# Optimization experiments

Hardware: AMD Instinct MI355X
Metric: run time of the kernel (lower is better)

## Reference

```python
import jax, jax.numpy as jnp
import numpy as np

B, S, D, H = 2, 2048, 2048, 16
HD = D // H


def setup_inputs() -> dict:
    key = jax.random.key(0)
    ks = jax.random.split(key, 9)
    scale = 0.02
    return {
        "x": jax.random.normal(ks[0], (B, S, D), dtype=jnp.float32),
        "wq_w": jax.random.normal(ks[1], (D, D), dtype=jnp.float32) * scale,
        "wq_b": jnp.zeros((D,), dtype=jnp.float32),
        "wk_w": jax.random.normal(ks[2], (D, D), dtype=jnp.float32) * scale,
        "wk_b": jnp.zeros((D,), dtype=jnp.float32),
        "wv_w": jax.random.normal(ks[3], (D, D), dtype=jnp.float32) * scale,
        "wv_b": jnp.zeros((D,), dtype=jnp.float32),
        "wo_w": jax.random.normal(ks[4], (D, D), dtype=jnp.float32) * scale,
        "wo_b": jnp.zeros((D,), dtype=jnp.float32),
    }


def reference(x, wq_w, wq_b, wk_w, wk_b, wv_w, wv_b, wo_w, wo_b):
    # torch Linear: y = x @ W.T + b
    q = x @ wq_w.T + wq_b  # [B,S,D]
    k = x @ wk_w.T + wk_b
    v = x @ wv_w.T + wv_b
    # [B,S,D] -> [B,H,S,HD]
    q = q.reshape(B, S, H, HD).transpose(0, 2, 1, 3)
    k = k.reshape(B, S, H, HD).transpose(0, 2, 1, 3)
    v = v.reshape(B, S, H, HD).transpose(0, 2, 1, 3)
    # scores [B,H,S,S], scaled by sqrt(d_dim) as in the original (not head_dim)
    scores = jnp.einsum("bhid,bhjd->bhij", q, k) / np.float32(np.sqrt(D))
    # faithful reproduction of the module's triu/transpose masking:
    m = jnp.swapaxes(jnp.triu(scores), -2, -1)  # lower-tri, zeros elsewhere
    p = jax.nn.softmax(m, axis=-2)              # softmax over dim=-2, zeros included
    a = jnp.swapaxes(jnp.triu(p), -2, -1)       # [B,H,S,S]
    attn = jnp.einsum("bhij,bhjd->bhid", a, v)  # [B,H,S,HD]
    concat = attn.transpose(0, 2, 1, 3).reshape(B, S, D)
    return concat @ wo_w.T + wo_b
```

## Files before the change

### kernel.cpp

```cpp
#include <hip/hip_runtime.h>

#define BB 2
#define SS 2048
#define DD 2048
#define HH 16
#define HDIM 128
#define MTOK (BB*SS)
#define BHH (BB*HH)
#define NCHUNK 16
#define QKN (2*DD)

typedef __attribute__((ext_vector_type(8))) __bf16 bf16x8;
typedef __attribute__((ext_vector_type(4))) float f32x4;
typedef __attribute__((ext_vector_type(8))) int i32x8;
typedef __attribute__((ext_vector_type(4))) int i32x4;

__device__ __forceinline__ unsigned short f2bf(float f) {
  unsigned u = __float_as_uint(f);
  u += 0x7FFFu + ((u >> 16) & 1u);
  return (unsigned short)(u >> 16);
}
__device__ __forceinline__ float bf2f(unsigned short s) {
  return __uint_as_float(((unsigned)s) << 16);
}
__device__ __forceinline__ unsigned char f2e4m3(float f) {
  int pk = __builtin_amdgcn_cvt_pk_fp8_f32(f, f, 0, false);
  return (unsigned char)(pk & 0xFF);
}

#define GLOAD_LDS16(src, dst)                                                   \
  __builtin_amdgcn_global_load_lds(                                             \
      (const void __attribute__((address_space(1)))*)(src),                     \
      (void __attribute__((address_space(3)))*)(dst), 16, 0, 0)

__global__ void cvt_x_dual(const float* __restrict__ in,
                           unsigned short* __restrict__ outb,
                           unsigned int* __restrict__ out8, int n4) {
  int i = blockIdx.x * blockDim.x + threadIdx.x;
  if (i < n4) {
    float4 v = ((const float4*)in)[i];
    ushort4 o;
    o.x = f2bf(v.x); o.y = f2bf(v.y); o.z = f2bf(v.z); o.w = f2bf(v.w);
    ((ushort4*)outb)[i] = o;
    int p0 = __builtin_amdgcn_cvt_pk_fp8_f32(v.x, v.y, 0, false);
    int p1 = __builtin_amdgcn_cvt_pk_fp8_f32(v.z, v.w, 0, false);
    out8[i] = (unsigned)(p0 & 0xFFFF) | ((unsigned)(p1 & 0xFFFF) << 16);
  }
}

__global__ void cvt_wqk8(const float* __restrict__ a, const float* __restrict__ b,
                         unsigned int* __restrict__ out) {
  int i = blockIdx.x * blockDim.x + threadIdx.x;
  int sel = i >> 20, r = i & 0xFFFFF;
  const float* src = sel == 0 ? a : b;
  float4 v = ((const float4*)src)[r];
  int p0 = __builtin_amdgcn_cvt_pk_fp8_f32(v.x, v.y, 0, false);
  int p1 = __builtin_amdgcn_cvt_pk_fp8_f32(v.z, v.w, 0, false);
  out[i] = (unsigned)(p0 & 0xFFFF) | ((unsigned)(p1 & 0xFFFF) << 16);
}

__global__ void cvt_w2bf(const float* __restrict__ a, const float* __restrict__ b,
                         unsigned short* __restrict__ out) {
  int i = blockIdx.x * blockDim.x + threadIdx.x;
  int sel = i >> 20, r = i & 0xFFFFF;
  const float* src = sel == 0 ? a : b;
  float4 v = ((const float4*)src)[r];
  ushort4 o;
  o.x = f2bf(v.x); o.y = f2bf(v.y); o.z = f2bf(v.z); o.w = f2bf(v.w);
  ((ushort4*)out)[i] = o;
}

__global__ void concat2(const float* __restrict__ a, const float* __restrict__ b,
                        float* __restrict__ out) {
  int i = blockIdx.x * blockDim.x + threadIdx.x;
  if (i < DD) { out[i] = a[i]; out[DD + i] = b[i]; }
}

template <bool OUT_BF16>
__global__ __launch_bounds__(256, 2) void gemm_bt(
    const __bf16* __restrict__ A, const __bf16* __restrict__ W,
    const float* __restrict__ bias, void* __restrict__ Cout,
    int M, int N, int K) {
  __shared__ __bf16 lA[128 * 32];
  __shared__ __bf16 lB[128 * 32];
  const int t = threadIdx.x;
  const int lane = t & 63, wave = t >> 6;
  const int quad = lane >> 4, l16 = lane & 15;
  const int m0 = blockIdx.y * 128, n0 = blockIdx.x * 128;
  const int wm = (wave & 1) * 64, wn = (wave >> 1) * 64;

  f32x4 acc[4][4] = {};

  for (int k0 = 0; k0 < K; k0 += 32) {
#pragma unroll
    for (int c = 0; c < 2; ++c) {
      int lin = c * 256 + t;
      int row = lin >> 2;
      int col = (lin & 3) * 8;
      const __bf16* srcA = A + (size_t)(m0 + row) * K + k0 + col;
      const __bf16* srcB = W + (size_t)(n0 + row) * K + k0 + col;
      GLOAD_LDS16(srcA, &lA[(c * 256 + wave * 64) * 8]);
      GLOAD_LDS16(srcB, &lB[(c * 256 + wave * 64) * 8]);
    }
    __syncthreads();
    bf16x8 af[4], bfr[4];
#pragma unroll
    for (int mt = 0; mt < 4; ++mt)
      af[mt] = *(const bf16x8*)&lA[(wm + mt * 16 + l16) * 32 + quad * 8];
#pragma unroll
    for (int nt = 0; nt < 4; ++nt)
      bfr[nt] = *(const bf16x8*)&lB[(wn + nt * 16 + l16) * 32 + quad * 8];
#pragma unroll
    for (int mt = 0; mt < 4; ++mt)
#pragma unroll
      for (int nt = 0; nt < 4; ++nt)
        acc[mt][nt] = __builtin_amdgcn_mfma_f32_16x16x32_bf16(af[mt], bfr[nt],
                                                              acc[mt][nt], 0, 0, 0);
    __syncthreads();
  }

#pragma unroll
  for (int mt = 0; mt < 4; ++mt) {
#pragma unroll
    for (int nt = 0; nt < 4; ++nt) {
      int col = n0 + wn + nt * 16 + l16;
      float bv = bias[col];
#pragma unroll
      for (int r = 0; r < 4; ++r) {
        int row = m0 + wm + mt * 16 + quad * 4 + r;
        float v = acc[mt][nt][r] + bv;
        if constexpr (OUT_BF16)
          ((unsigned short*)Cout)[(size_t)row * N + col] = f2bf(v);
        else
          ((float*)Cout)[(size_t)row * N + col] = v;
      }
    }
  }
}

__global__ __launch_bounds__(256, 2) void gemm_qk_fp8(
    const unsigned char* __restrict__ A8, const unsigned char* __restrict__ W8,
    const float* __restrict__ bias, unsigned char* __restrict__ Cout,
    int M, int N, int K) {
  __shared__ unsigned char lA[128 * 128];
  __shared__ unsigned char lB[128 * 128];
  const int t = threadIdx.x;
  const int lane = t & 63, wave = t >> 6;
  const int quad = lane >> 4, l16 = lane & 15;
  const int m0 = blockIdx.y * 128, n0 = blockIdx.x * 128;
  const int wm = (wave & 1) * 64, wn = (wave >> 1) * 64;
  const int p0 = (2 * quad) ^ (l16 & 7);

  f32x4 acc[4][4] = {};

  for (int k0 = 0; k0 < K; k0 += 128) {
#pragma unroll
    for (int c = 0; c < 4; ++c) {
      int lin = c * 256 + t;
      int row = lin >> 3;
      int ch = lin & 7;
      int sch = ch ^ (row & 7);
      const unsigned char* srcA = A8 + (size_t)(m0 + row) * K + k0 + sch * 16;
      const unsigned char* srcB = W8 + (size_t)(n0 + row) * K + k0 + sch * 16;
      GLOAD_LDS16(srcA, &lA[(c * 256 + wave * 64) * 16]);
      GLOAD_LDS16(srcB, &lB[(c * 256 + wave * 64) * 16]);
    }
    __syncthreads();
    i32x8 af[4];
#pragma unroll
    for (int mt = 0; mt < 4; ++mt) {
      int ra = (wm + mt * 16 + l16) * 128 + p0 * 16;
      ((i32x4*)&af[mt])[0] = *(const i32x4*)&lA[ra];
      ((i32x4*)&af[mt])[1] = *(const i32x4*)&lA[ra ^ 16];
    }
#pragma unroll
    for (int nt = 0; nt < 4; ++nt) {
      int rb = (wn + nt * 16 + l16) * 128 + p0 * 16;
      i32x8 bfr;
      ((i32x4*)&bfr)[0] = *(const i32x4*)&lB[rb];
      ((i32x4*)&bfr)[1] = *(const i32x4*)&lB[rb ^ 16];
#pragma unroll
      for (int mt = 0; mt < 4; ++mt)
        acc[mt][nt] = __builtin_amdgcn_mfma_scale_f32_16x16x128_f8f6f4(
            af[mt], bfr, acc[mt][nt], 0 , 0 ,
            0, 127 , 0, 127 );
    }
    __syncthreads();
  }

#pragma unroll
  for (int mt = 0; mt < 4; ++mt) {
#pragma unroll
    for (int nt = 0; nt < 4; ++nt) {
      int col = n0 + wn + nt * 16 + l16;
      float bv = bias[col];
#pragma unroll
      for (int r = 0; r < 4; ++r) {
        int row = m0 + wm + mt * 16 + quad * 4 + r;
        Cout[(size_t)row * N + col] = f2e4m3(acc[mt][nt][r] + bv);
      }
    }
  }
}

__global__ __launch_bounds__(256, 4) void qk_rowsum8(
    const unsigned char* __restrict__ q8, const unsigned char* __restrict__ k8,
    float* __restrict__ denomA, float* __restrict__ denomB,
    float* __restrict__ diag) {
  __shared__ unsigned char lK[2][128 * 128];
  __shared__ float redS[4][64];
  __shared__ float redD[4][64];
  const int t = threadIdx.x;
  const int lane = t & 63, wave = t >> 6;
  const int quad = lane >> 4, l16 = lane & 15;
  const int bh = blockIdx.y;
  const int b = bh >> 4, h = bh & 15;
  const int pair = blockIdx.x >> 1;
  const int half = blockIdx.x & 1;
  const float C = 0.03187935771f;
  const f32x4 fz = {0.f, 0.f, 0.f, 0.f};

  int soff[4];
#pragma unroll
  for (int c = 0; c < 4; ++c) {
    int L = c * 256 + t;
    int row = L >> 3, p = L & 7;
    soff[c] = row * QKN + ((p ^ (row & 7)) * 16);
  }
  const int p0 = (2 * quad) ^ (l16 & 7);
  int bo[2];
#pragma unroll
  for (int nt = 0; nt < 2; ++nt)
    bo[nt] = (wave * 32 + nt * 16 + l16) * 128 + p0 * 16;

  const unsigned char* kbase = k8 + (size_t)(b * SS) * QKN + h * HDIM;

  for (int sub = 0; sub < 2; ++sub) {
    const int tile = (sub == 0) ? pair : 31 - pair;
    const int i0 = tile * 64;
    const int jbase = i0 & ~127;
    const int ntile = (SS - jbase) >> 7;

    i32x8 af[4];
    {
      const unsigned char* qbase =
          q8 + (size_t)(b * SS + i0 + l16) * QKN + h * HDIM + quad * 32;
#pragma unroll
      for (int mt = 0; mt < 4; ++mt)
        af[mt] = *(const i32x8*)(qbase + (size_t)(mt * 16) * QKN);
    }

    float rowacc[4][4] = {};

    int kidx = half;
    if (kidx < ntile) {
      {
        const unsigned char* src = kbase + (size_t)(jbase + kidx * 128) * QKN;
#pragma unroll
        for (int c = 0; c < 4; ++c)
          GLOAD_LDS16(src + soff[c], &lK[0][(c * 256 + wave * 64) * 16]);
      }
      asm volatile("s_waitcnt vmcnt(0)" ::: "memory");
      __syncthreads();
      int cur = 0;
      for (; kidx < ntile; kidx += 2, cur ^= 1) {
        if (kidx + 2 < ntile) {
          const unsigned char* src =
              kbase + (size_t)(jbase + (kidx + 2) * 128) * QKN;
#pragma unroll
          for (int c = 0; c < 4; ++c)
            GLOAD_LDS16(src + soff[c], &lK[cur ^ 1][(c * 256 + wave * 64) * 16]);
        }
        const unsigned char* lkc = lK[cur];
        const int j0 = jbase + kidx * 128;
        if (kidx == 0) {
          float dloc[4][4] = {};
#pragma unroll
          for (int nt = 0; nt < 2; ++nt) {
            i32x8 bf;
            ((i32x4*)&bf)[0] = *(const i32x4*)(lkc + bo[nt]);
            ((i32x4*)&bf)[1] = *(const i32x4*)(lkc + (bo[nt] ^ 16));
            f32x4 acc[4];
#pragma unroll
            for (int mt = 0; mt < 4; ++mt)
              acc[mt] = __builtin_amdgcn_mfma_scale_f32_16x16x128_f8f6f4(
                  af[mt], bf, fz, 0, 0, 0, 127, 0, 127);
            const int colg = j0 + wave * 32 + nt * 16 + l16;
#pragma unroll
            for (int mt = 0; mt < 4; ++mt)
#pragma unroll
              for (int r = 0; r < 4; ++r) {
                int rg = i0 + mt * 16 + quad * 4 + r;
                float e = (colg >= rg)
                              ? __builtin_amdgcn_exp2f(acc[mt][r] * C) : 0.f;
                rowacc[mt][r] += e;
                if (colg == rg) dloc[mt][r] = e;
              }
          }
#pragma unroll
          for (int mt = 0; mt < 4; ++mt)
#pragma unroll
            for (int r = 0; r < 4; ++r) {
              float d = dloc[mt][r];
#pragma unroll
              for (int off = 1; off < 16; off <<= 1) d += __shfl_xor(d, off, 64);
              if (l16 == 0) redD[wave][mt * 16 + quad * 4 + r] = d;
            }
        } else {
#pragma unroll
          for (int nt = 0; nt < 2; ++nt) {
            i32x8 bf;
            ((i32x4*)&bf)[0] = *(const i32x4*)(lkc + bo[nt]);
            ((i32x4*)&bf)[1] = *(const i32x4*)(lkc + (bo[nt] ^ 16));
            f32x4 acc[4];
#pragma unroll
            for (int mt = 0; mt < 4; ++mt)
              acc[mt] = __builtin_amdgcn_mfma_scale_f32_16x16x128_f8f6f4(
                  af[mt], bf, fz, 0, 0, 0, 127, 0, 127);
#pragma unroll
            for (int mt = 0; mt < 4; ++mt)
#pragma unroll
              for (int r = 0; r < 4; ++r)
                rowacc[mt][r] += __builtin_amdgcn_exp2f(acc[mt][r] * C);
          }
        }
        asm volatile("s_waitcnt vmcnt(0)" ::: "memory");
        __syncthreads();
      }
    }

    __syncthreads();
#pragma unroll
    for (int mt = 0; mt < 4; ++mt)
#pragma unroll
      for (int r = 0; r < 4; ++r) {
        float s = rowacc[mt][r];
#pragma unroll
        for (int off = 1; off < 16; off <<= 1) s += __shfl_xor(s, off, 64);
        if (l16 == 0) redS[wave][mt * 16 + quad * 4 + r] = s;
      }
    __syncthreads();
    if (t < 64) {
      const int rg = i0 + t;
      float s = redS[0][t] + redS[1][t] + redS[2][t] + redS[3][t];
      if (half == 0) {
        denomA[bh * SS + rg] = (float)rg + s;
        diag[bh * SS + rg] = redD[0][t] + redD[1][t] + redD[2][t] + redD[3][t];
      } else {
        denomB[bh * SS + rg] = s;
      }
    }
  }
}

__global__ void scan_pass1(const __bf16* __restrict__ v0,
                           float* __restrict__ csum) {
  int blk = blockIdx.x;
  int bh = blk >> 4, c = blk & 15;
  int b = bh >> 4, h = bh & 15;
  int t = threadIdx.x;
  int rs = t >> 4, dg = t & 15;
  const unsigned short* base = (const unsigned short*)v0 +
      (size_t)(b * SS + c * 128 + rs * 8) * DD + h * HDIM + dg * 8;
  float s[8] = {0.f, 0.f, 0.f, 0.f, 0.f, 0.f, 0.f, 0.f};
#pragma unroll
  for (int i = 0; i < 8; ++i) {
    uint4 u = *(const uint4*)(base + (size_t)i * DD);
    const unsigned short* us = (const unsigned short*)&u;
#pragma unroll
    for (int j = 0; j < 8; ++j) s[j] += bf2f(us[j]);
  }
  __shared__ float red[16 * 128];
#pragma unroll
  for (int j = 0; j < 8; ++j) red[rs * 128 + dg * 8 + j] = s[j];
  __syncthreads();
  for (int st = 8; st >= 1; st >>= 1) {
    if (rs < st) {
#pragma unroll
      for (int j = 0; j < 8; ++j)
        red[rs * 128 + dg * 8 + j] += red[(rs + st) * 128 + dg * 8 + j];
    }
    __syncthreads();
  }
  if (rs == 0) {
#pragma unroll
    for (int j = 0; j < 8; ++j)
      csum[(size_t)blk * 128 + dg * 8 + j] = red[dg * 8 + j];
  }
}

__global__ void scan_pass2(const __bf16* __restrict__ v0,
                           const float* __restrict__ csum,
                           const float* __restrict__ denomA,
                           const float* __restrict__ denomB,
                           const float* __restrict__ diag,
                           unsigned short* __restrict__ ctx) {
  int blk = blockIdx.x;
  int bh = blk >> 4, c = blk & 15;
  int b = bh >> 4, h = bh & 15;
  int t = threadIdx.x;
  int rs = t >> 4, dg = t & 15;
  const unsigned short* vbase = (const unsigned short*)v0 +
      (size_t)(b * SS + c * 128 + rs * 8) * DD + h * HDIM + dg * 8;
  float vrow[8][8];
  float ls[8] = {0.f, 0.f, 0.f, 0.f, 0.f, 0.f, 0.f, 0.f};
#pragma unroll
  for (int i = 0; i < 8; ++i) {
    uint4 u = *(const uint4*)(vbase + (size_t)i * DD);
    const unsigned short* us = (const unsigned short*)&u;
#pragma unroll
    for (int j = 0; j < 8; ++j) {
      vrow[i][j] = bf2f(us[j]);
      ls[j] += vrow[i][j];
    }
  }
  __shared__ float red[16 * 128];
#pragma unroll
  for (int j = 0; j < 8; ++j) red[rs * 128 + dg * 8 + j] = ls[j];
  __syncthreads();

  float pre[8] = {0.f, 0.f, 0.f, 0.f, 0.f, 0.f, 0.f, 0.f};
  for (int cc = 0; cc < c; ++cc) {
    const float* cp = csum + (size_t)(bh * 16 + cc) * 128 + dg * 8;
#pragma unroll
    for (int j = 0; j < 8; ++j) pre[j] += cp[j];
  }
  for (int ss2 = 0; ss2 < rs; ++ss2) {
#pragma unroll
    for (int j = 0; j < 8; ++j) pre[j] += red[ss2 * 128 + dg * 8 + j];
  }

  int row0 = c * 128 + rs * 8;
  unsigned short* obase =
      ctx + (size_t)(b * SS + row0) * DD + h * HDIM + dg * 8;
  const float* dnA = denomA + bh * SS + row0;
  const float* dnB = denomB + bh * SS + row0;
  const float* dgp = diag + bh * SS + row0;
#pragma unroll
  for (int i = 0; i < 8; ++i) {
    float inv = 1.0f / (dnA[i] + dnB[i]);
    float dv = dgp[i];
    unsigned short o[8];
#pragma unroll
    for (int j = 0; j < 8; ++j) {
      float val = (pre[j] + dv * vrow[i][j]) * inv;
      o[j] = f2bf(val);
      pre[j] += vrow[i][j];
    }
    *(uint4*)(obase + (size_t)i * DD) = *(const uint4*)o;
  }
}

extern "C" void kernel_launch(void* const* d_in, const int* in_sizes, int n_in,
                              void* d_out, int out_size, void* d_ws, size_t ws_size,
                              hipStream_t stream) {
  (void)in_sizes; (void)n_in; (void)out_size; (void)ws_size;
  const float* x    = (const float*)d_in[0];
  const float* wq_w = (const float*)d_in[1];
  const float* wq_b = (const float*)d_in[2];
  const float* wk_w = (const float*)d_in[3];
  const float* wk_b = (const float*)d_in[4];
  const float* wv_w = (const float*)d_in[5];
  const float* wv_b = (const float*)d_in[6];
  const float* wo_w = (const float*)d_in[7];
  const float* wo_b = (const float*)d_in[8];

  char* ws = (char*)d_ws;
  size_t off = 0;
  auto alloc = [&](size_t bytes) {
    char* p = ws + off;
    off += (bytes + 255) & ~(size_t)255;
    return p;
  };
  unsigned short* xb   = (unsigned short*)alloc((size_t)MTOK * DD * 2);
  unsigned char*  x8   = (unsigned char*)alloc((size_t)MTOK * DD);
  unsigned char*  wqk8 = (unsigned char*)alloc((size_t)2 * DD * DD);
  unsigned short* wvo  = (unsigned short*)alloc((size_t)2 * DD * DD * 2);
  unsigned char*  qk8  = (unsigned char*)alloc((size_t)MTOK * QKN);
  unsigned short* v    = (unsigned short*)alloc((size_t)MTOK * DD * 2);
  unsigned short* ctx  = (unsigned short*)alloc((size_t)MTOK * DD * 2);
  float* biasqk = (float*)alloc((size_t)2 * DD * 4);
  float* denomA = (float*)alloc((size_t)BHH * SS * 4);
  float* denomB = (float*)alloc((size_t)BHH * SS * 4);
  float* diag   = (float*)alloc((size_t)BHH * SS * 4);
  float* csum   = (float*)alloc((size_t)BHH * NCHUNK * 128 * 4);

  {
    int n4 = MTOK * DD / 4;
    cvt_x_dual<<<n4 / 256, 256, 0, stream>>>(x, xb, (unsigned int*)x8, n4);
    cvt_wqk8<<<(2 << 20) / 256, 256, 0, stream>>>(wq_w, wk_w, (unsigned int*)wqk8);
    cvt_w2bf<<<(2 << 20) / 256, 256, 0, stream>>>(wv_w, wo_w, wvo);
    concat2<<<(DD + 255) / 256, 256, 0, stream>>>(wq_b, wk_b, biasqk);
  }

  gemm_qk_fp8<<<dim3(QKN / 128, MTOK / 128), 256, 0, stream>>>(
      x8, wqk8, biasqk, qk8, MTOK, QKN, DD);

  gemm_bt<true><<<dim3(DD / 128, MTOK / 128), 256, 0, stream>>>(
      (const __bf16*)xb, (const __bf16*)wvo, wv_b, v, MTOK, DD, DD);

  qk_rowsum8<<<dim3(32, BHH), 256, 0, stream>>>(
      qk8,
      qk8 + DD,
      denomA, denomB, diag);

  scan_pass1<<<BHH * NCHUNK, 256, 0, stream>>>((const __bf16*)v, csum);
  scan_pass2<<<BHH * NCHUNK, 256, 0, stream>>>((const __bf16*)v, csum,
                                               denomA, denomB, diag, ctx);

  gemm_bt<false><<<dim3(DD / 128, MTOK / 128), 256, 0, stream>>>(
      (const __bf16*)ctx, (const __bf16*)(wvo + (size_t)DD * DD), wo_b,
      d_out, MTOK, DD, DD);
}
```

Before: 349.4 us.

## Rewrite bf16 GEMM with 256x128 tiles, double-buffered LDS and XOR swizzle

Replaces the 128x128, 256-thread bf16 GEMM with a 512-thread kernel that computes 256x128 tiles over a BK=64 K step. The kernel double-buffers LDS, prefetching the next K tile while the current one is consumed. It also XOR-swizzles the LDS layout to avoid bank conflicts, remaps block IDs for L2 locality, and raises wave priority around the MFMA bursts. The aim is to hide global-load latency and cut LDS conflicts, at the cost of 96KB of LDS per block, which allows only one block per CU.

```diff
diff --git a/kernel.cpp b/kernel.cpp
--- a/kernel.cpp
+++ b/kernel.cpp
@@ -32,6 +32,12 @@
   __builtin_amdgcn_global_load_lds(                                             \
       (const void __attribute__((address_space(1)))*)(src),                     \
       (void __attribute__((address_space(3)))*)(dst), 16, 0, 0)
+
+__device__ __forceinline__ void barrier_raw() {
+  asm volatile("" ::: "memory");
+  __builtin_amdgcn_s_barrier();
+  asm volatile("" ::: "memory");
+}
 
 __global__ void cvt_x_dual(const float* __restrict__ in,
                            unsigned short* __restrict__ outb,
@@ -77,46 +83,105 @@
 }
 
 template <bool OUT_BF16>
-__global__ __launch_bounds__(256, 2) void gemm_bt(
+__global__ __launch_bounds__(512, 1) void gemm_bt8(
     const __bf16* __restrict__ A, const __bf16* __restrict__ W,
     const float* __restrict__ bias, void* __restrict__ Cout,
     int M, int N, int K) {
-  __shared__ __bf16 lA[128 * 32];
-  __shared__ __bf16 lB[128 * 32];
+  __shared__ unsigned char lds[2][49152];
   const int t = threadIdx.x;
   const int lane = t & 63, wave = t >> 6;
   const int quad = lane >> 4, l16 = lane & 15;
-  const int m0 = blockIdx.y * 128, n0 = blockIdx.x * 128;
-  const int wm = (wave & 1) * 64, wn = (wave >> 1) * 64;
+  const int bid = blockIdx.x;
+  const int swz = (bid & 7) * 32 + (bid >> 3);
+  const int m0 = (swz >> 4) * 256;
+  const int n0 = (swz & 15) * 128;
+  const int wm = (wave >> 1) * 64;
+  const int wn = (wave & 1) * 64;
+
+  const __bf16* sA[4];
+#pragma unroll
+  for (int c = 0; c < 4; ++c) {
+    int L = c * 512 + t;
+    int row = L >> 3, p = L & 7;
+    sA[c] = A + (size_t)(m0 + row) * K + ((p ^ (row & 7)) * 8);
+  }
+  const __bf16* sB[2];
+#pragma unroll
+  for (int c = 0; c < 2; ++c) {
+    int L = c * 512 + t;
+    int row = L >> 3, p = L & 7;
+    sB[c] = W + (size_t)(n0 + row) * K + ((p ^ (row & 7)) * 8);
+  }
+  const int phk0 = (quad ^ (l16 & 7)) * 16;
+  const int phk1 = ((4 + quad) ^ (l16 & 7)) * 16;
 
   f32x4 acc[4][4] = {};
 
-  for (int k0 = 0; k0 < K; k0 += 32) {
-#pragma unroll
-    for (int c = 0; c < 2; ++c) {
-      int lin = c * 256 + t;
-      int row = lin >> 2;
-      int col = (lin & 3) * 8;
-      const __bf16* srcA = A + (size_t)(m0 + row) * K + k0 + col;
-      const __bf16* srcB = W + (size_t)(n0 + row) * K + k0 + col;
-      GLOAD_LDS16(srcA, &lA[(c * 256 + wave * 64) * 8]);
-      GLOAD_LDS16(srcB, &lB[(c * 256 + wave * 64) * 8]);
-    }
-    __syncthreads();
-    bf16x8 af[4], bfr[4];
-#pragma unroll
-    for (int mt = 0; mt < 4; ++mt)
-      af[mt] = *(const bf16x8*)&lA[(wm + mt * 16 + l16) * 32 + quad * 8];
-#pragma unroll
-    for (int nt = 0; nt < 4; ++nt)
-      bfr[nt] = *(const bf16x8*)&lB[(wn + nt * 16 + l16) * 32 + quad * 8];
-#pragma unroll
-    for (int mt = 0; mt < 4; ++mt)
+  const int NT = K >> 6;
+
+#pragma unroll
+  for (int c = 0; c < 4; ++c)
+    GLOAD_LDS16(sA[c], &lds[0][c * 8192 + wave * 1024]);
+#pragma unroll
+  for (int c = 0; c < 2; ++c)
+    GLOAD_LDS16(sB[c], &lds[0][32768 + c * 8192 + wave * 1024]);
+
+  for (int tt = 0; tt < NT; ++tt) {
+    const int cur = tt & 1;
+    const bool pf = (tt + 1 < NT);
+    const int k1 = (tt + 1) << 6;
+
+    if (pf) {
+#pragma unroll
+      for (int c = 0; c < 4; ++c)
+        GLOAD_LDS16(sA[c] + k1, &lds[cur ^ 1][c * 8192 + wave * 1024]);
+      asm volatile("s_waitcnt vmcnt(4)" ::: "memory");
+    } else {
+      asm volatile("s_waitcnt vmcnt(0)" ::: "memory");
+    }
+    barrier_raw();
+    {
+      bf16x8 af[4], bfv[4];
+#pragma unroll
+      for (int mt = 0; mt < 4; ++mt)
+        af[mt] = *(const bf16x8*)&lds[cur][(wm + mt * 16 + l16) * 128 + phk0];
 #pragma unroll
       for (int nt = 0; nt < 4; ++nt)
-        acc[mt][nt] = __builtin_amdgcn_mfma_f32_16x16x32_bf16(af[mt], bfr[nt],
-                                                              acc[mt][nt], 0, 0, 0);
-    __syncthreads();
+        bfv[nt] = *(const bf16x8*)&lds[cur][32768 + (wn + nt * 16 + l16) * 128 + phk0];
+      __builtin_amdgcn_s_setprio(1);
+#pragma unroll
+      for (int mt = 0; mt < 4; ++mt)
+#pragma unroll
+        for (int nt = 0; nt < 4; ++nt)
+          acc[mt][nt] = __builtin_amdgcn_mfma_f32_16x16x32_bf16(
+              af[mt], bfv[nt], acc[mt][nt], 0, 0, 0);
+      __builtin_amdgcn_s_setprio(0);
+    }
+
+    if (pf) {
+#pragma unroll
+      for (int c = 0; c < 2; ++c)
+        GLOAD_LDS16(sB[c] + k1, &lds[cur ^ 1][32768 + c * 8192 + wave * 1024]);
+    }
+    barrier_raw();
+    {
+      bf16x8 af[4], bfv[4];
+#pragma unroll
+      for (int mt = 0; mt < 4; ++mt)
+        af[mt] = *(const bf16x8*)&lds[cur][(wm + mt * 16 + l16) * 128 + phk1];
+#pragma unroll
+      for (int nt = 0; nt < 4; ++nt)
+        bfv[nt] = *(const bf16x8*)&lds[cur][32768 + (wn + nt * 16 + l16) * 128 + phk1];
+      __builtin_amdgcn_s_setprio(1);
+#pragma unroll
+      for (int mt = 0; mt < 4; ++mt)
+#pragma unroll
+        for (int nt = 0; nt < 4; ++nt)
+          acc[mt][nt] = __builtin_amdgcn_mfma_f32_16x16x32_bf16(
+              af[mt], bfv[nt], acc[mt][nt], 0, 0, 0);
+      __builtin_amdgcn_s_setprio(0);
+    }
+    barrier_raw();
   }
 
 #pragma unroll
@@ -496,7 +561,7 @@
   gemm_qk_fp8<<<dim3(QKN / 128, MTOK / 128), 256, 0, stream>>>(
       x8, wqk8, biasqk, qk8, MTOK, QKN, DD);
 
-  gemm_bt<true><<<dim3(DD / 128, MTOK / 128), 256, 0, stream>>>(
+  gemm_bt8<true><<<(MTOK / 256) * (DD / 128), 512, 0, stream>>>(
       (const __bf16*)xb, (const __bf16*)wvo, wv_b, v, MTOK, DD, DD);
 
   qk_rowsum8<<<dim3(32, BHH), 256, 0, stream>>>(
@@ -508,7 +573,7 @@
   scan_pass2<<<BHH * NCHUNK, 256, 0, stream>>>((const __bf16*)v, csum,
                                                denomA, denomB, diag, ctx);
 
-  gemm_bt<false><<<dim3(DD / 128, MTOK / 128), 256, 0, stream>>>(
+  gemm_bt8<false><<<(MTOK / 256) * (DD / 128), 512, 0, stream>>>(
       (const __bf16*)ctx, (const __bf16*)(wvo + (size_t)DD * DD), wo_b,
       d_out, MTOK, DD, DD);
 }
```

New measurement: 316.7 us. -9.4%, faster.
